# Performance work log

Measured on AMD Instinct MI355X. Metric: run time of the kernel, lower is better.

Reference implementation:

```python
import jax, jax.numpy as jnp
import numpy as np

E = 8          # num_experts
K = 2          # top_k
CAPF = 1.25    # capacity_factor
DIM = 512
HID = 2048     # int(dim * mlp_ratio)


def setup_inputs() -> dict:
    key = jax.random.key(0)
    ks = jax.random.split(key, 5)
    s = 0.02
    x = jax.random.normal(ks[0], (8, 2048, DIM), jnp.float32)
    Wr = jax.random.normal(ks[1], (E, DIM), jnp.float32) * s          # router weight (no bias)
    W1 = jax.random.normal(ks[2], (E, HID, DIM), jnp.float32) * s     # fc1 weights per expert
    b1 = jnp.zeros((E, HID), jnp.float32)
    W2 = jax.random.normal(ks[3], (E, DIM, HID), jnp.float32) * s     # fc2 weights per expert
    b2 = jnp.zeros((E, DIM), jnp.float32)
    return {"x": x, "Wr": Wr, "W1": W1, "b1": b1, "W2": W2, "b2": b2}


def _capacity_keep(top_w, top_idx, cap):
    """For each (slot, expert), keep only the `cap` highest-weight tokens.
    top_w, top_idx: [T, K]. Returns bool keep mask [T, K]."""
    def per_slot(w, idx):
        order = jnp.argsort(-w)                       # tokens sorted by weight desc
        idx_sorted = idx[order]                       # [T] expert id in sorted order
        oh = jax.nn.one_hot(idx_sorted, E, dtype=jnp.int32)
        rank = jnp.cumsum(oh, axis=0) - 1             # rank within each expert
        r = jnp.take_along_axis(rank, idx_sorted[:, None], axis=1)[:, 0]
        keep_sorted = r < cap
        return jnp.zeros(w.shape[0], bool).at[order].set(keep_sorted)
    return jax.vmap(per_slot, in_axes=(1, 1), out_axes=1)(top_w, top_idx)


def reference(x, Wr, W1, b1, W2, b2):
    b, n, d = x.shape
    T = b * n
    flat = x.reshape(T, d)

    # Router: softmax in fp32 then cast back
    logits = flat @ Wr.T                                            # [T, E]
    probs = jax.nn.softmax(logits.astype(jnp.float32), axis=-1).astype(flat.dtype)
    top_w, top_idx = jax.lax.top_k(probs, K)                        # [T, K]
    top_w = top_w / (jnp.sum(top_w, axis=-1, keepdims=True) + 1e-8)

    # Capacity-limited drop, then renormalize
    cap = max(1, int(CAPF * T * K / E))
    keep = _capacity_keep(top_w, top_idx, cap)
    top_w = jnp.where(keep, top_w, 0.0)
    top_w = top_w / jnp.clip(jnp.sum(top_w, axis=-1, keepdims=True), 1e-8, None)

    # Combine weight per (token, expert): scatter-add top_w into dense [T, E]
    rows = jnp.arange(T)[:, None]
    w_te = jnp.zeros((T, E), flat.dtype).at[rows, top_idx].add(top_w)

    # Per-expert MLP, weighted combine (w_te is 0 for unassigned/dropped pairs)
    out = jnp.zeros_like(flat)
    for e in range(E):
        h = jax.nn.gelu(flat @ W1[e].T + b1[e], approximate=False)  # [T, HID]
        y = h @ W2[e].T + b2[e]                                     # [T, D]
        out = out + w_te[:, e:e + 1] * y

    # Load-balancing aux loss
    load = jnp.sum(w_te, axis=0) / T
    importance = probs.mean(0)
    aux = jnp.sum(importance * load * float(E))
    return out.reshape(b, n, d), aux
```

## Files before the change

### kernel.cpp

```cpp
#include <hip/hip_runtime.h>
#include <hip/hip_bf16.h>
#include <math.h>

#define DIM 512
#define HID 2048
#define NE  8
#define CSTRIDE 32
#define CVTB 1024

typedef __attribute__((ext_vector_type(8))) short short8;
typedef __attribute__((ext_vector_type(4))) float f32x4;
typedef unsigned short ushort_t;

static __device__ __forceinline__ ushort_t f2bf(float f) {
    unsigned int x = __builtin_bit_cast(unsigned int, f);
    unsigned int lsb = (x >> 16) & 1u;
    x += 0x7fffu + lsb;
    return (ushort_t)(x >> 16);
}
static __device__ __forceinline__ float bf2f(ushort_t u) {
    unsigned int x = ((unsigned int)u) << 16;
    return __builtin_bit_cast(float, x);
}

static __device__ __forceinline__ float fast_gelu(float v) {
    float z = v * fmaf(0.071354816f, v * v, 1.5957691f);
    return v * __builtin_amdgcn_rcpf(1.f + __expf(-z));
}

static __device__ __forceinline__ void gld16(const void* g, void* l) {
    __builtin_amdgcn_global_load_lds(
        (const __attribute__((address_space(1))) void*)g,
        (__attribute__((address_space(3))) void*)l,
        16, 0, 0);
}

__global__ __launch_bounds__(256) void k_init(
    const float* __restrict__ W1, ushort_t* __restrict__ W1b, int n1,
    const float* __restrict__ W2, ushort_t* __restrict__ W2b, int n2,
    const float* __restrict__ x, const float* __restrict__ Wr,
    ushort_t* __restrict__ xb, float* __restrict__ probs,
    int* __restrict__ tidx, float* __restrict__ tw, int T)
{
    if (blockIdx.x < CVTB) {
        int i = blockIdx.x * 256 + threadIdx.x;
        int stride = CVTB * 256;
        int n4a = n1 >> 2, n4b = n2 >> 2;
        for (int j = i; j < n4a; j += stride) {
            float4 v = ((const float4*)W1)[j];
            ushort4 o;
            o.x = f2bf(v.x); o.y = f2bf(v.y); o.z = f2bf(v.z); o.w = f2bf(v.w);
            ((ushort4*)W1b)[j] = o;
        }
        for (int j = i; j < n4b; j += stride) {
            float4 v = ((const float4*)W2)[j];
            ushort4 o;
            o.x = f2bf(v.x); o.y = f2bf(v.y); o.z = f2bf(v.z); o.w = f2bf(v.w);
            ((ushort4*)W2b)[j] = o;
        }
        return;
    }
    int lane = threadIdx.x & 63;
    int t = (blockIdx.x - CVTB) * 4 + (threadIdx.x >> 6);
    if (t >= T) return;
    const float* xr = x + (size_t)t * DIM;
    double acc[NE];
#pragma unroll
    for (int e = 0; e < NE; e++) acc[e] = 0.0;
    for (int i = lane; i < DIM; i += 64) {
        float xv = xr[i];
        xb[(size_t)t * DIM + i] = f2bf(xv);
        double xd = (double)xv;
#pragma unroll
        for (int e = 0; e < NE; e++) acc[e] += xd * (double)Wr[e * DIM + i];
    }
#pragma unroll
    for (int e = 0; e < NE; e++) {
#pragma unroll
        for (int off = 32; off > 0; off >>= 1) acc[e] += __shfl_xor(acc[e], off);
    }
    double mx = acc[0];
#pragma unroll
    for (int e = 1; e < NE; e++) mx = fmax(mx, acc[e]);
    double p[NE], sum = 0.0;
#pragma unroll
    for (int e = 0; e < NE; e++) { p[e] = exp(acc[e] - mx); sum += p[e]; }
    float pr[NE];
#pragma unroll
    for (int e = 0; e < NE; e++) pr[e] = (float)(p[e] / sum);
    if (lane < NE) probs[(size_t)t * NE + lane] = pr[lane];
    if (lane == 0) {
        int i1 = 0; float b1v = pr[0];
#pragma unroll
        for (int e = 1; e < NE; e++) if (pr[e] > b1v) { b1v = pr[e]; i1 = e; }
        int i2 = -1; float b2v = -1.f;
#pragma unroll
        for (int e = 0; e < NE; e++) if (e != i1 && pr[e] > b2v) { b2v = pr[e]; i2 = e; }
        float s2 = b1v + b2v + 1e-8f;
        tidx[t * 2] = i1; tidx[t * 2 + 1] = i2;
        tw[t * 2] = b1v / s2; tw[t * 2 + 1] = b2v / s2;
    }
}

__global__ __launch_bounds__(256) void k_hist(const int* __restrict__ tidx,
                                              int* __restrict__ cnt, int T) {
    __shared__ int h[16];
    if (threadIdx.x < 16) h[threadIdx.x] = 0;
    __syncthreads();
    int stride = gridDim.x * blockDim.x;
    for (int t = blockIdx.x * blockDim.x + threadIdx.x; t < T; t += stride) {
        atomicAdd(&h[tidx[t * 2]], 1);
        atomicAdd(&h[8 + tidx[t * 2 + 1]], 1);
    }
    __syncthreads();
    if (threadIdx.x < 16 && h[threadIdx.x] != 0)
        atomicAdd(&cnt[threadIdx.x * CSTRIDE], h[threadIdx.x]);
}

__global__ __launch_bounds__(256) void k_post(const int* __restrict__ tidx,
        const float* __restrict__ tw, const int* __restrict__ cnt,
        const float* __restrict__ probs, int* __restrict__ lcnt,
        int* __restrict__ ltok, int* __restrict__ pos, float* __restrict__ tw2,
        float* __restrict__ partial, int T, int cap, int capM)
{
    __shared__ int h[NE];
    __shared__ int base[NE];
    __shared__ float red[256 * 16];
    if (threadIdx.x < NE) h[threadIdx.x] = 0;
    __syncthreads();
    int t = blockIdx.x * blockDim.x + threadIdx.x;
    float wkn[2] = {0.f, 0.f};
    int myE[2] = {-1, -1};
    int myp[2] = {0, 0};
    if (t < T) {
        float wk[2]; int es[2];
#pragma unroll
        for (int s = 0; s < 2; s++) {
            int e = tidx[t * 2 + s];
            float w = tw[t * 2 + s];
            es[s] = e; wk[s] = w;
            if (cnt[(s * NE + e) * CSTRIDE] > cap) {
                int rank = 0;
                for (int t2 = 0; t2 < T; t2++) {
                    if (tidx[t2 * 2 + s] == e) {
                        float w2 = tw[t2 * 2 + s];
                        if (w2 > w || (w2 == w && t2 < t)) rank++;
                    }
                }
                if (rank >= cap) wk[s] = 0.f;
            }
        }
        float denom = fmaxf(wk[0] + wk[1], 1e-8f);
#pragma unroll
        for (int s = 0; s < 2; s++) {
            wkn[s] = wk[s] / denom;
            tw2[t * 2 + s] = wkn[s];
            if (wkn[s] != 0.f) {
                myE[s] = es[s];
                myp[s] = atomicAdd(&h[es[s]], 1);
            }
        }
    }
    __syncthreads();
    if (threadIdx.x < NE)
        base[threadIdx.x] = (h[threadIdx.x] != 0)
            ? atomicAdd(&lcnt[threadIdx.x * CSTRIDE], h[threadIdx.x]) : 0;
    __syncthreads();
    float imp[NE], ld[NE];
#pragma unroll
    for (int e = 0; e < NE; e++) { imp[e] = 0.f; ld[e] = 0.f; }
    if (t < T) {
#pragma unroll
        for (int s = 0; s < 2; s++) {
            if (myE[s] >= 0) {
                int p = base[myE[s]] + myp[s];
                ltok[myE[s] * capM + p] = t;
                pos[t * 2 + s] = (myE[s] << 20) | p;
                ld[myE[s]] += wkn[s];
            } else {
                pos[t * 2 + s] = -1;
            }
        }
#pragma unroll
        for (int e = 0; e < NE; e++) imp[e] = probs[(size_t)t * NE + e];
    }
#pragma unroll
    for (int e = 0; e < NE; e++) {
        red[threadIdx.x * 16 + e] = imp[e];
        red[threadIdx.x * 16 + 8 + e] = ld[e];
    }
    __syncthreads();
    for (int off = 128; off > 0; off >>= 1) {
        if (threadIdx.x < off) {
#pragma unroll
            for (int j = 0; j < 16; j++)
                red[threadIdx.x * 16 + j] += red[(threadIdx.x + off) * 16 + j];
        }
        __syncthreads();
    }
    if (threadIdx.x < 16) partial[blockIdx.x * 16 + threadIdx.x] = red[threadIdx.x];
}

__global__ void k_tail(const int* __restrict__ lcnt, int* __restrict__ loff,
                       const float* __restrict__ partial, float* __restrict__ outaux,
                       int nb, int T)
{
    __shared__ float s[16];
    if (threadIdx.x == 0) {
        int o = 0;
        for (int e = 0; e < NE; e++) {
            loff[e] = o;
            o += ((lcnt[e * CSTRIDE] + 127) >> 7) << 7;
        }
        loff[NE] = o;
    }
    if (threadIdx.x < 16) {
        float a = 0.f;
        for (int b = 0; b < nb; b++) a += partial[b * 16 + threadIdx.x];
        s[threadIdx.x] = a;
    }
    __syncthreads();
    if (threadIdx.x == 0) {
        float invT = 1.f / (float)T;
        float aux = 0.f;
        for (int e = 0; e < NE; e++)
            aux += (s[e] * invT) * (s[8 + e] * invT) * (float)NE;
        outaux[0] = aux;
    }
}

__global__ __launch_bounds__(256, 2) void k_fc1(
    const ushort_t* __restrict__ xb, const ushort_t* __restrict__ W1b,
    const float* __restrict__ b1, const int* __restrict__ lcnt,
    const int* __restrict__ loff, const int* __restrict__ ltok,
    ushort_t* __restrict__ hbuf, int capM)
{
    int bx = blockIdx.x;
    int e  = bx & 7;
    int r  = bx >> 3;
    int mt = r >> 4;
    int nt = r & 15;
    int cnt = lcnt[e * CSTRIDE];
    if (cnt > capM) cnt = capM;
    int m0 = mt * 128;
    if (m0 >= cnt) return;
    int n0 = nt * 128;
    const int* toks = ltok + e * capM;
    int hrow0 = loff[e] + m0;
    const ushort_t* Bsrc = W1b + (size_t)e * HID * DIM;

    __shared__ char smem[65536];
    char* As0 = smem;          char* Bs0 = smem + 16384;
    char* As1 = smem + 32768;  char* Bs1 = smem + 49152;

    int tid = threadIdx.x;
    int wave = tid >> 6, lane = tid & 63;
    int wm = wave >> 1, wn = wave & 1;

    const char* aSrc[4]; const char* bSrc[4]; int ldst[4];
#pragma unroll
    for (int i = 0; i < 4; i++) {
        int c = tid + 256 * i;
        int row = c >> 3, cc = c & 7;
        int scc = cc ^ (row & 7);
        int gr = m0 + row;
        int tok = toks[gr < cnt ? gr : (cnt - 1)];
        aSrc[i] = (const char*)(xb + (size_t)tok * DIM + scc * 8);
        bSrc[i] = (const char*)(Bsrc + (size_t)(n0 + row) * DIM + scc * 8);
        ldst[i] = (i * 256 + wave * 64) * 16;
    }

    const float* b1e = b1 + e * HID;
    int nbase0 = n0 + wn * 64 + (lane >> 4) * 4;
    f32x4 acc[4][4];
#pragma unroll
    for (int nf = 0; nf < 4; nf++) {
        float4 bias4 = *(const float4*)(b1e + nbase0 + nf * 16);
        f32x4 bi = (f32x4){bias4.x, bias4.y, bias4.z, bias4.w};
#pragma unroll
        for (int mf = 0; mf < 4; mf++) acc[mf][nf] = bi;
    }

    int aRow = wm * 64 + (lane & 15);
    int bRow = wn * 64 + (lane & 15);
    int kq = lane >> 4;
    int swz0 = (kq ^ (lane & 7)) << 4;
    int swz1 = ((4 + kq) ^ (lane & 7)) << 4;
    int aoff[2] = { aRow * 128 + swz0, aRow * 128 + swz1 };
    int boff[2] = { bRow * 128 + swz0, bRow * 128 + swz1 };

    auto STAGE = [&](int kofs, char* A, char* B) {
#pragma unroll
        for (int i = 0; i < 4; i++) {
            gld16(aSrc[i] + kofs, A + ldst[i]);
            gld16(bSrc[i] + kofs, B + ldst[i]);
        }
    };
    auto COMPUTE = [&](const char* A, const char* B) {
#pragma unroll
        for (int kk = 0; kk < 2; kk++) {
            short8 af[4], bfr[4];
#pragma unroll
            for (int mf = 0; mf < 4; mf++)
                af[mf] = *(const short8*)(A + aoff[kk] + mf * 2048);
#pragma unroll
            for (int nf = 0; nf < 4; nf++)
                bfr[nf] = *(const short8*)(B + boff[kk] + nf * 2048);
#pragma unroll
            for (int mf = 0; mf < 4; mf++)
#pragma unroll
                for (int nf = 0; nf < 4; nf++)
                    acc[mf][nf] = __builtin_amdgcn_mfma_f32_16x16x32_bf16(bfr[nf], af[mf], acc[mf][nf], 0, 0, 0);
        }
    };

    const int NT = DIM / 64;
    STAGE(0, As0, Bs0);
#pragma unroll
    for (int t = 0; t < NT; t++) {
        char* Ac = (t & 1) ? As1 : As0;
        char* Bc = (t & 1) ? Bs1 : Bs0;
        if (t + 1 < NT) {
            STAGE((t + 1) * 128, (t & 1) ? As0 : As1, (t & 1) ? Bs0 : Bs1);
            asm volatile("s_waitcnt vmcnt(8)" ::: "memory");
        } else {
            asm volatile("s_waitcnt vmcnt(0)" ::: "memory");
        }
        __builtin_amdgcn_s_barrier();
        __builtin_amdgcn_sched_barrier(0);
        COMPUTE(Ac, Bc);
        __builtin_amdgcn_sched_barrier(0);
        __builtin_amdgcn_s_barrier();
    }

    int mlocal = wm * 64 + (lane & 15);
#pragma unroll
    for (int mf = 0; mf < 4; mf++) {
        int mrow = mlocal + mf * 16;
        bool valid = (m0 + mrow) < cnt;
        ushort_t* dst = hbuf + (size_t)(hrow0 + mrow) * HID;
#pragma unroll
        for (int nf = 0; nf < 4; nf++) {
            int nc = nbase0 + nf * 16;
            ushort4 o;
            o.x = f2bf(fast_gelu(acc[mf][nf][0]));
            o.y = f2bf(fast_gelu(acc[mf][nf][1]));
            o.z = f2bf(fast_gelu(acc[mf][nf][2]));
            o.w = f2bf(fast_gelu(acc[mf][nf][3]));
            if (valid) *(ushort4*)(dst + nc) = o;
        }
    }
}

__global__ __launch_bounds__(256, 2) void k_fc2(
    const ushort_t* __restrict__ hbuf, const ushort_t* __restrict__ W2b,
    const float* __restrict__ b2, const int* __restrict__ lcnt,
    const int* __restrict__ loff, ushort_t* __restrict__ ybuf, int capM)
{
    int bx = blockIdx.x;
    int e  = bx & 7;
    int r  = bx >> 3;
    int mt = r >> 2;
    int nt = r & 3;
    int cnt = lcnt[e * CSTRIDE];
    if (cnt > capM) cnt = capM;
    int m0 = mt * 128;
    if (m0 >= cnt) return;
    int n0 = nt * 128;
    int hrow0 = loff[e] + m0;
    const ushort_t* Bsrc = W2b + (size_t)e * DIM * HID;

    __shared__ char smem[65536];
    char* As0 = smem;          char* Bs0 = smem + 16384;
    char* As1 = smem + 32768;  char* Bs1 = smem + 49152;

    int tid = threadIdx.x;
    int wave = tid >> 6, lane = tid & 63;
    int wm = wave >> 1, wn = wave & 1;

    const char* aSrc[4]; const char* bSrc[4]; int ldst[4];
#pragma unroll
    for (int i = 0; i < 4; i++) {
        int c = tid + 256 * i;
        int row = c >> 3, cc = c & 7;
        int scc = cc ^ (row & 7);
        aSrc[i] = (const char*)(hbuf + (size_t)(hrow0 + row) * HID + scc * 8);
        bSrc[i] = (const char*)(Bsrc + (size_t)(n0 + row) * HID + scc * 8);
        ldst[i] = (i * 256 + wave * 64) * 16;
    }

    const float* b2e = b2 + e * DIM;
    int nbase0 = n0 + wn * 64 + (lane >> 4) * 4;
    f32x4 acc[4][4];
#pragma unroll
    for (int nf = 0; nf < 4; nf++) {
        float4 bias4 = *(const float4*)(b2e + nbase0 + nf * 16);
        f32x4 bi = (f32x4){bias4.x, bias4.y, bias4.z, bias4.w};
#pragma unroll
        for (int mf = 0; mf < 4; mf++) acc[mf][nf] = bi;
    }

    int aRow = wm * 64 + (lane & 15);
    int bRow = wn * 64 + (lane & 15);
    int kq = lane >> 4;
    int swz0 = (kq ^ (lane & 7)) << 4;
    int swz1 = ((4 + kq) ^ (lane & 7)) << 4;
    int aoff[2] = { aRow * 128 + swz0, aRow * 128 + swz1 };
    int boff[2] = { bRow * 128 + swz0, bRow * 128 + swz1 };

    auto STAGE = [&](int kofs, char* A, char* B) {
#pragma unroll
        for (int i = 0; i < 4; i++) {
            gld16(aSrc[i] + kofs, A + ldst[i]);
            gld16(bSrc[i] + kofs, B + ldst[i]);
        }
    };
    auto COMPUTE = [&](const char* A, const char* B) {
#pragma unroll
        for (int kk = 0; kk < 2; kk++) {
            short8 af[4], bfr[4];
#pragma unroll
            for (int mf = 0; mf < 4; mf++)
                af[mf] = *(const short8*)(A + aoff[kk] + mf * 2048);
#pragma unroll
            for (int nf = 0; nf < 4; nf++)
                bfr[nf] = *(const short8*)(B + boff[kk] + nf * 2048);
#pragma unroll
            for (int mf = 0; mf < 4; mf++)
#pragma unroll
                for (int nf = 0; nf < 4; nf++)
                    acc[mf][nf] = __builtin_amdgcn_mfma_f32_16x16x32_bf16(bfr[nf], af[mf], acc[mf][nf], 0, 0, 0);
        }
    };

    const int NT = HID / 64;
    STAGE(0, As0, Bs0);
#pragma unroll
    for (int t = 0; t < NT; t++) {
        char* Ac = (t & 1) ? As1 : As0;
        char* Bc = (t & 1) ? Bs1 : Bs0;
        if (t + 1 < NT) {
            STAGE((t + 1) * 128, (t & 1) ? As0 : As1, (t & 1) ? Bs0 : Bs1);
            asm volatile("s_waitcnt vmcnt(8)" ::: "memory");
        } else {
            asm volatile("s_waitcnt vmcnt(0)" ::: "memory");
        }
        __builtin_amdgcn_s_barrier();
        __builtin_amdgcn_sched_barrier(0);
        COMPUTE(Ac, Bc);
        __builtin_amdgcn_sched_barrier(0);
        __builtin_amdgcn_s_barrier();
    }

    int mlocal = wm * 64 + (lane & 15);
#pragma unroll
    for (int mf = 0; mf < 4; mf++) {
        int mrow = mlocal + mf * 16;
        bool valid = (m0 + mrow) < cnt;
        ushort_t* dst = ybuf + (size_t)(hrow0 + mrow) * DIM;
#pragma unroll
        for (int nf = 0; nf < 4; nf++) {
            int nc = nbase0 + nf * 16;
            ushort4 o;
            o.x = f2bf(acc[mf][nf][0]);
            o.y = f2bf(acc[mf][nf][1]);
            o.z = f2bf(acc[mf][nf][2]);
            o.w = f2bf(acc[mf][nf][3]);
            if (valid) *(ushort4*)(dst + nc) = o;
        }
    }
}

__global__ __launch_bounds__(256) void k_comb(const ushort_t* __restrict__ ybuf,
    const float* __restrict__ tw2, const int* __restrict__ pos,
    const int* __restrict__ loff, float* __restrict__ out, int T, int capM)
{
    int wv = threadIdx.x >> 6, lane = threadIdx.x & 63;
#pragma unroll
    for (int half = 0; half < 2; half++) {
        int t = blockIdx.x * 8 + wv * 2 + half;
        if (t >= T) continue;
        float o[8];
#pragma unroll
        for (int j = 0; j < 8; j++) o[j] = 0.f;
#pragma unroll
        for (int s = 0; s < 2; s++) {
            int pk = pos[t * 2 + s];
            if (pk >= 0) {
                float w = tw2[t * 2 + s];
                int e = pk >> 20, p = pk & 0xFFFFF;
                int row = loff[e] + p;
                short8 y = *(const short8*)(ybuf + (size_t)row * DIM + lane * 8);
#pragma unroll
                for (int j = 0; j < 8; j++) o[j] += w * bf2f((ushort_t)y[j]);
            }
        }
        float4* dst = (float4*)(out + (size_t)t * DIM + lane * 8);
        dst[0] = (float4){o[0], o[1], o[2], o[3]};
        dst[1] = (float4){o[4], o[5], o[6], o[7]};
    }
}

extern "C" void kernel_launch(void* const* d_in, const int* in_sizes, int n_in,
                              void* d_out, int out_size, void* d_ws, size_t ws_size,
                              hipStream_t stream)
{
    const float* x  = (const float*)d_in[0];
    const float* Wr = (const float*)d_in[1];
    const float* W1 = (const float*)d_in[2];
    const float* b1 = (const float*)d_in[3];
    const float* W2 = (const float*)d_in[4];
    const float* b2 = (const float*)d_in[5];
    float* out = (float*)d_out;

    int T = in_sizes[0] / DIM;
    int cap = (int)(1.25 * (double)T * 2.0 / 8.0);
    if (cap < 1) cap = 1;
    int capM = 2 * cap; if (capM > T) capM = T;
    int mtmax = (capM + 127) / 128;
    int nposts = (T + 255) / 256;

    char* w = (char*)d_ws;
    size_t off = 0;
    auto alloc = [&](size_t bytes) {
        char* p = w + off;
        off = (off + bytes + 255) & ~(size_t)255;
        return p;
    };
    size_t ybrows = (size_t)T * 2 + NE * 128;
    size_t ybbytes = ybrows * DIM * 2;
    ushort_t* ybuf = (ushort_t*)w;
    ushort_t* xb   = (ushort_t*)alloc((size_t)T * DIM * 2);
    ushort_t* W1b  = (ushort_t*)alloc((size_t)NE * HID * DIM * 2);
    if (off < ybbytes) off = (ybbytes + 255) & ~(size_t)255;
    ushort_t* W2b  = (ushort_t*)alloc((size_t)NE * DIM * HID * 2);
    ushort_t* hbuf = (ushort_t*)alloc(ybrows * HID * 2);
    float* probs   = (float*)alloc((size_t)T * NE * 4);
    int*   tidx    = (int*)alloc((size_t)T * 2 * 4);
    float* tw      = (float*)alloc((size_t)T * 2 * 4);
    float* tw2     = (float*)alloc((size_t)T * 2 * 4);
    int*   pos     = (int*)alloc((size_t)T * 2 * 4);
    int*   cnt     = (int*)alloc(16 * CSTRIDE * 4);
    int*   lcnt    = (int*)alloc(NE * CSTRIDE * 4);
    int*   loff    = (int*)alloc((NE + 1) * 4);
    int*   ltok    = (int*)alloc((size_t)NE * capM * 4);
    float* partial = (float*)alloc((size_t)nposts * 16 * 4);

    (void)hipMemsetAsync(cnt, 0, 16 * CSTRIDE * 4, stream);
    (void)hipMemsetAsync(lcnt, 0, NE * CSTRIDE * 4, stream);

    int nrb = (T + 3) / 4;
    k_init<<<CVTB + nrb, 256, 0, stream>>>(W1, W1b, NE * HID * DIM,
                                           W2, W2b, NE * DIM * HID,
                                           x, Wr, xb, probs, tidx, tw, T);
    k_hist<<<64, 256, 0, stream>>>(tidx, cnt, T);
    k_post<<<nposts, 256, 0, stream>>>(tidx, tw, cnt, probs, lcnt, ltok, pos, tw2,
                                       partial, T, cap, capM);
    k_tail<<<1, 64, 0, stream>>>(lcnt, loff, partial, out + (size_t)T * DIM, nposts, T);

    k_fc1<<<NE * mtmax * (HID / 128), 256, 0, stream>>>(
        xb, W1b, b1, lcnt, loff, ltok, hbuf, capM);
    k_fc2<<<NE * mtmax * (DIM / 128), 256, 0, stream>>>(
        hbuf, W2b, b2, lcnt, loff, ybuf, capM);
    k_comb<<<(T + 7) / 8, 256, 0, stream>>>(ybuf, tw2, pos, loff, out, T, capM);
}
```

Before: 258.2 us.

## Fuse weighted expert combine into fc2 epilogue with global atomic adds

The separate combine kernel and the bf16 intermediate expert-output buffer are removed. k_post now stores each kept (expert, slot) pair's renormalized weight alongside its token index. The fc2 epilogue scales its fp32 accumulators by that weight and atomically adds them straight into the zeroed output rows. This avoids writing and re-reading the per-expert output buffer and saves one kernel launch. The cost is an extra memset of the output and many scattered fp32 global atomics, which may be poorly coalesced and contend in L2.

```diff
diff --git a/kernel.cpp b/kernel.cpp
--- a/kernel.cpp
+++ b/kernel.cpp
@@ -17,10 +17,6 @@
     unsigned int lsb = (x >> 16) & 1u;
     x += 0x7fffu + lsb;
     return (ushort_t)(x >> 16);
-}
-static __device__ __forceinline__ float bf2f(ushort_t u) {
-    unsigned int x = ((unsigned int)u) << 16;
-    return __builtin_bit_cast(float, x);
 }
 
 static __device__ __forceinline__ float fast_gelu(float v) {
@@ -120,7 +116,7 @@
 __global__ __launch_bounds__(256) void k_post(const int* __restrict__ tidx,
         const float* __restrict__ tw, const int* __restrict__ cnt,
         const float* __restrict__ probs, int* __restrict__ lcnt,
-        int* __restrict__ ltok, int* __restrict__ pos, float* __restrict__ tw2,
+        int* __restrict__ ltok, float* __restrict__ lwb,
         float* __restrict__ partial, int T, int cap, int capM)
 {
     __shared__ int h[NE];
@@ -154,7 +150,6 @@
 #pragma unroll
         for (int s = 0; s < 2; s++) {
             wkn[s] = wk[s] / denom;
-            tw2[t * 2 + s] = wkn[s];
             if (wkn[s] != 0.f) {
                 myE[s] = es[s];
                 myp[s] = atomicAdd(&h[es[s]], 1);
@@ -175,10 +170,8 @@
             if (myE[s] >= 0) {
                 int p = base[myE[s]] + myp[s];
                 ltok[myE[s] * capM + p] = t;
-                pos[t * 2 + s] = (myE[s] << 20) | p;
+                lwb[myE[s] * capM + p] = wkn[s];
                 ld[myE[s]] += wkn[s];
-            } else {
-                pos[t * 2 + s] = -1;
             }
         }
 #pragma unroll
@@ -355,7 +348,8 @@
 __global__ __launch_bounds__(256, 2) void k_fc2(
     const ushort_t* __restrict__ hbuf, const ushort_t* __restrict__ W2b,
     const float* __restrict__ b2, const int* __restrict__ lcnt,
-    const int* __restrict__ loff, ushort_t* __restrict__ ybuf, int capM)
+    const int* __restrict__ loff, const int* __restrict__ ltok,
+    const float* __restrict__ lwb, float* __restrict__ out, int capM)
 {
     int bx = blockIdx.x;
     int e  = bx & 7;
@@ -452,52 +446,24 @@
         __builtin_amdgcn_s_barrier();
     }
 
+    const int* toks = ltok + e * capM;
+    const float* lws = lwb + e * capM;
     int mlocal = wm * 64 + (lane & 15);
 #pragma unroll
     for (int mf = 0; mf < 4; mf++) {
-        int mrow = mlocal + mf * 16;
-        bool valid = (m0 + mrow) < cnt;
-        ushort_t* dst = ybuf + (size_t)(hrow0 + mrow) * DIM;
-#pragma unroll
-        for (int nf = 0; nf < 4; nf++) {
-            int nc = nbase0 + nf * 16;
-            ushort4 o;
-            o.x = f2bf(acc[mf][nf][0]);
-            o.y = f2bf(acc[mf][nf][1]);
-            o.z = f2bf(acc[mf][nf][2]);
-            o.w = f2bf(acc[mf][nf][3]);
-            if (valid) *(ushort4*)(dst + nc) = o;
-        }
-    }
-}
-
-__global__ __launch_bounds__(256) void k_comb(const ushort_t* __restrict__ ybuf,
-    const float* __restrict__ tw2, const int* __restrict__ pos,
-    const int* __restrict__ loff, float* __restrict__ out, int T, int capM)
-{
-    int wv = threadIdx.x >> 6, lane = threadIdx.x & 63;
-#pragma unroll
-    for (int half = 0; half < 2; half++) {
-        int t = blockIdx.x * 8 + wv * 2 + half;
-        if (t >= T) continue;
-        float o[8];
-#pragma unroll
-        for (int j = 0; j < 8; j++) o[j] = 0.f;
-#pragma unroll
-        for (int s = 0; s < 2; s++) {
-            int pk = pos[t * 2 + s];
-            if (pk >= 0) {
-                float w = tw2[t * 2 + s];
-                int e = pk >> 20, p = pk & 0xFFFFF;
-                int row = loff[e] + p;
-                short8 y = *(const short8*)(ybuf + (size_t)row * DIM + lane * 8);
-#pragma unroll
-                for (int j = 0; j < 8; j++) o[j] += w * bf2f((ushort_t)y[j]);
+        int gr = m0 + mlocal + mf * 16;
+        if (gr < cnt) {
+            int tok = toks[gr];
+            float wgt = lws[gr];
+            float* orow = out + (size_t)tok * DIM;
+#pragma unroll
+            for (int nf = 0; nf < 4; nf++) {
+                int nc = nbase0 + nf * 16;
+#pragma unroll
+                for (int j = 0; j < 4; j++)
+                    atomicAdd(&orow[nc + j], wgt * acc[mf][nf][j]);
             }
         }
-        float4* dst = (float4*)(out + (size_t)t * DIM + lane * 8);
-        dst[0] = (float4){o[0], o[1], o[2], o[3]};
-        dst[1] = (float4){o[4], o[5], o[6], o[7]};
     }
 }
 
@@ -527,25 +493,22 @@
         off = (off + bytes + 255) & ~(size_t)255;
         return p;
     };
-    size_t ybrows = (size_t)T * 2 + NE * 128;
-    size_t ybbytes = ybrows * DIM * 2;
-    ushort_t* ybuf = (ushort_t*)w;
+    size_t hrows = (size_t)T * 2 + NE * 128;
     ushort_t* xb   = (ushort_t*)alloc((size_t)T * DIM * 2);
     ushort_t* W1b  = (ushort_t*)alloc((size_t)NE * HID * DIM * 2);
-    if (off < ybbytes) off = (ybbytes + 255) & ~(size_t)255;
     ushort_t* W2b  = (ushort_t*)alloc((size_t)NE * DIM * HID * 2);
-    ushort_t* hbuf = (ushort_t*)alloc(ybrows * HID * 2);
+    ushort_t* hbuf = (ushort_t*)alloc(hrows * HID * 2);
     float* probs   = (float*)alloc((size_t)T * NE * 4);
     int*   tidx    = (int*)alloc((size_t)T * 2 * 4);
     float* tw      = (float*)alloc((size_t)T * 2 * 4);
-    float* tw2     = (float*)alloc((size_t)T * 2 * 4);
-    int*   pos     = (int*)alloc((size_t)T * 2 * 4);
     int*   cnt     = (int*)alloc(16 * CSTRIDE * 4);
     int*   lcnt    = (int*)alloc(NE * CSTRIDE * 4);
     int*   loff    = (int*)alloc((NE + 1) * 4);
     int*   ltok    = (int*)alloc((size_t)NE * capM * 4);
+    float* lwb     = (float*)alloc((size_t)NE * capM * 4);
     float* partial = (float*)alloc((size_t)nposts * 16 * 4);
 
+    (void)hipMemsetAsync(out, 0, (size_t)out_size * 4, stream);
     (void)hipMemsetAsync(cnt, 0, 16 * CSTRIDE * 4, stream);
     (void)hipMemsetAsync(lcnt, 0, NE * CSTRIDE * 4, stream);
 
@@ -554,13 +517,12 @@
                                            W2, W2b, NE * DIM * HID,
                                            x, Wr, xb, probs, tidx, tw, T);
     k_hist<<<64, 256, 0, stream>>>(tidx, cnt, T);
-    k_post<<<nposts, 256, 0, stream>>>(tidx, tw, cnt, probs, lcnt, ltok, pos, tw2,
+    k_post<<<nposts, 256, 0, stream>>>(tidx, tw, cnt, probs, lcnt, ltok, lwb,
                                        partial, T, cap, capM);
     k_tail<<<1, 64, 0, stream>>>(lcnt, loff, partial, out + (size_t)T * DIM, nposts, T);
 
     k_fc1<<<NE * mtmax * (HID / 128), 256, 0, stream>>>(
         xb, W1b, b1, lcnt, loff, ltok, hbuf, capM);
     k_fc2<<<NE * mtmax * (DIM / 128), 256, 0, stream>>>(
-        hbuf, W2b, b2, lcnt, loff, ybuf, capM);
-    k_comb<<<(T + 7) / 8, 256, 0, stream>>>(ybuf, tw2, pos, loff, out, T, capM);
-}
+        hbuf, W2b, b2, lcnt, loff, ltok, lwb, out, capM);
+}
```

New measurement: 435.5 us. 1.69x slower.
